# Optimization experiments

Measured on AMD Instinct MI355X. Metric: run time of the kernel, lower is better.

Reference implementation:

```python
import jax, jax.numpy as jnp
import numpy as np

N_NODES = 40000
N_EDGES = 640000
IN_CH = 11
HID = 128
OUT_CH = 1
NUM_LEVELS = 2


def _lin(x, w, b):
    # torch nn.Linear: w is [out, in]
    return x @ w.T + b


def _conv(x, src, dst, w1, b1, w2, b2, w3, b3):
    # Reconstructed MLMPNNConv forward: embed, then NUM_LEVELS rounds of
    # scatter-add message passing (message = x_j), concat levels, project.
    h = jax.nn.relu(_lin(x, w1, b1))  # [N, HID]
    outs = []
    for _ in range(NUM_LEVELS):
        agg = jax.ops.segment_sum(h[src], dst, num_segments=N_NODES)  # gather + scatter-add
        h = jax.nn.relu(_lin(agg, w2, b2))
        outs.append(h)
    return _lin(jnp.concatenate(outs, axis=-1), w3, b3)  # [N, out]


def setup_inputs() -> dict:
    key = jax.random.key(0)
    ks = jax.random.split(key, 16)
    d = {}
    d["x"] = jax.random.normal(ks[0], (N_NODES, IN_CH), dtype=jnp.float32)
    d["edge_index"] = jax.random.randint(ks[1], (2, N_EDGES), 0, N_NODES, dtype=jnp.int32)
    s = 0.05
    # conv 0: lin1 IN->HID, lin2 HID->HID, lin3 2*HID->HID
    d["c0_w1"] = jax.random.normal(ks[2], (HID, IN_CH)) * s
    d["c0_b1"] = jnp.zeros((HID,), jnp.float32)
    d["c0_w2"] = jax.random.normal(ks[3], (HID, HID)) * s
    d["c0_b2"] = jnp.zeros((HID,), jnp.float32)
    d["c0_w3"] = jax.random.normal(ks[4], (HID, HID * NUM_LEVELS)) * s
    d["c0_b3"] = jnp.zeros((HID,), jnp.float32)
    # conv 1: lin1 HID->HID
    d["c1_w1"] = jax.random.normal(ks[5], (HID, HID)) * s
    d["c1_b1"] = jnp.zeros((HID,), jnp.float32)
    d["c1_w2"] = jax.random.normal(ks[6], (HID, HID)) * s
    d["c1_b2"] = jnp.zeros((HID,), jnp.float32)
    d["c1_w3"] = jax.random.normal(ks[7], (HID, HID * NUM_LEVELS)) * s
    d["c1_b3"] = jnp.zeros((HID,), jnp.float32)
    # head
    d["f_w1"] = jax.random.normal(ks[8], (HID, HID)) * s
    d["f_b1"] = jnp.zeros((HID,), jnp.float32)
    d["f_w2"] = jax.random.normal(ks[9], (OUT_CH, HID)) * s
    d["f_b2"] = jnp.zeros((OUT_CH,), jnp.float32)
    return d


def reference(x, edge_index,
              c0_w1, c0_b1, c0_w2, c0_b2, c0_w3, c0_b3,
              c1_w1, c1_b1, c1_w2, c1_b2, c1_w3, c1_b3,
              f_w1, f_b1, f_w2, f_b2):
    src, dst = edge_index[0], edge_index[1]
    h = _conv(x, src, dst, c0_w1, c0_b1, c0_w2, c0_b2, c0_w3, c0_b3)
    h = _conv(h, src, dst, c1_w1, c1_b1, c1_w2, c1_b2, c1_w3, c1_b3)
    h = jax.nn.relu(_lin(h, f_w1, f_b1))
    return _lin(h, f_w2, f_b2)  # [N, 1]
```

## Files before the change

kernel.cpp:

```cpp
#include <hip/hip_runtime.h>
#include <hip/hip_fp16.h>

#define NN 40000
#define NE 640000
#define HID 128
#define SCAN_BLK ((NN + 255) / 256)

typedef __attribute__((ext_vector_type(8)))  short short8;
typedef __attribute__((ext_vector_type(4)))  short short4v;
typedef __attribute__((ext_vector_type(16))) float floatx16;
typedef unsigned int uint;

__device__ __forceinline__ short f2bf(float f) {
    union { float f; unsigned u; } c; c.f = f;
    unsigned u = c.u;
    unsigned r = (u + 0x7FFF + ((u >> 16) & 1)) >> 16;
    return (short)r;
}
__device__ __forceinline__ float bf2f(short h) {
    union { unsigned u; float f; } c;
    c.u = ((unsigned)(unsigned short)h) << 16;
    return c.f;
}
__device__ __forceinline__ float2 h2f2(uint u) {
    union { uint u; __half2 h; } c; c.u = u;
    return __half22float2(c.h);
}
__device__ __forceinline__ void splits(float f, short* hi, short* lo) {
    short h = f2bf(f);
    *hi = h;
    *lo = f2bf(f - bf2f(h));
}
__device__ __forceinline__ void unpack8(uint4 a, uint4 b, short8* h, short8* l) {
    short8 H, L;
    H[0] = (short)(a.x >> 16); L[0] = (short)a.x;
    H[1] = (short)(a.y >> 16); L[1] = (short)a.y;
    H[2] = (short)(a.z >> 16); L[2] = (short)a.z;
    H[3] = (short)(a.w >> 16); L[3] = (short)a.w;
    H[4] = (short)(b.x >> 16); L[4] = (short)b.x;
    H[5] = (short)(b.y >> 16); L[5] = (short)b.y;
    H[6] = (short)(b.z >> 16); L[6] = (short)b.z;
    H[7] = (short)(b.w >> 16); L[7] = (short)b.w;
    *h = H; *l = L;
}

__device__ __forceinline__ int wswz(int o, int k) {
    int chunk = k >> 4, half = (k >> 3) & 1, j = k & 7;
    int ct = o >> 5, m31 = o & 31;
    int lane = half * 32 + m31;
    return (((chunk * 4 + ct) * 64 + lane) * 8 + j);
}

#define ACCH(u, A)                                      \
    { float2 f0 = h2f2(u.x), f1 = h2f2(u.y);            \
      A.x += f0.x; A.y += f0.y; A.z += f1.x; A.w += f1.y; }

__global__ __launch_bounds__(256, 4) void fused_gather_lin_kernel(
    const __half* __restrict__ h, const int* __restrict__ row_ptr,
    const int* __restrict__ esrc, const uint* __restrict__ Wq,
    const float* __restrict__ bias, __half* __restrict__ out)
{
    __shared__ short sAh[4096];
    __shared__ short sAl[4096];
    const int t  = threadIdx.x;
    const int r0 = blockIdx.x * 32;
    const int c4 = t & 31;
    const int sub = c4 >> 1;
    const int j0  = (c4 & 1) * 4;
    const uint2* hp = (const uint2*)h;

    for (int p = 0; p < 4; ++p) {
        const int nl   = p * 8 + (t >> 5);
        const int node = r0 + nl;
        const int lo = row_ptr[node], hi = row_ptr[node + 1];
        float4 a = make_float4(0,0,0,0), b = make_float4(0,0,0,0);
        float4 c = make_float4(0,0,0,0), d = make_float4(0,0,0,0);
        int e = lo;
        for (; e + 4 <= hi; e += 4) {
            int s0 = esrc[e], s1 = esrc[e+1], s2 = esrc[e+2], s3 = esrc[e+3];
            uint2 u0 = hp[(size_t)s0 * 32 + c4];
            uint2 u1 = hp[(size_t)s1 * 32 + c4];
            uint2 u2 = hp[(size_t)s2 * 32 + c4];
            uint2 u3 = hp[(size_t)s3 * 32 + c4];
            ACCH(u0, a); ACCH(u1, b); ACCH(u2, c); ACCH(u3, d);
        }
        for (; e < hi; ++e) {
            int s0 = esrc[e];
            uint2 u0 = hp[(size_t)s0 * 32 + c4];
            ACCH(u0, a);
        }
        float vx = (a.x + b.x) + (c.x + d.x);
        float vy = (a.y + b.y) + (c.y + d.y);
        float vz = (a.z + b.z) + (c.z + d.z);
        float vw = (a.w + b.w) + (c.w + d.w);
        short4v Hq, Lq;
        short hh, ll;
        splits(vx, &hh, &ll); Hq.x = hh; Lq.x = ll;
        splits(vy, &hh, &ll); Hq.y = hh; Lq.y = ll;
        splits(vz, &hh, &ll); Hq.z = hh; Lq.z = ll;
        splits(vw, &hh, &ll); Hq.w = hh; Lq.w = ll;
        const int off = sub * 256 + nl * 8 + j0;
        *(short4v*)(sAh + off) = Hq;
        *(short4v*)(sAl + off) = Lq;
    }
    __syncthreads();

    const int wv   = t >> 6;
    const int lane = t & 63;
    const int m31  = lane & 31;
    const int half = lane >> 5;
    floatx16 acc;
    #pragma unroll
    for (int i = 0; i < 16; ++i) acc[i] = 0.f;
    #pragma unroll
    for (int c = 0; c < 8; ++c) {
        short8 ah = *(const short8*)(sAh + (c * 2 + half) * 256 + m31 * 8);
        short8 al = *(const short8*)(sAl + (c * 2 + half) * 256 + m31 * 8);
        const uint* wr = Wq + ((size_t)(c * 4 + wv) * 64 + lane) * 8;
        uint4 w0 = *(const uint4*)(wr);
        uint4 w1 = *(const uint4*)(wr + 4);
        short8 bh, bl;
        unpack8(w0, w1, &bh, &bl);
        acc = __builtin_amdgcn_mfma_f32_32x32x16_bf16(ah, bh, acc, 0, 0, 0);
        acc = __builtin_amdgcn_mfma_f32_32x32x16_bf16(al, bh, acc, 0, 0, 0);
        acc = __builtin_amdgcn_mfma_f32_32x32x16_bf16(ah, bl, acc, 0, 0, 0);
    }
    const int col = wv * 32 + m31;
    const float bb = bias[col];
    #pragma unroll
    for (int reg = 0; reg < 16; ++reg) {
        int row = (reg & 3) + 8 * (reg >> 2) + 4 * half;
        float v = fmaxf(acc[reg] + bb, 0.f);
        out[(size_t)(r0 + row) * HID + col] = __float2half(v);
    }
}

template<int PHASES, bool RELU>
__global__ __launch_bounds__(256, 4) void lin32_kernel(
    const __half* __restrict__ X0, const __half* __restrict__ X1,
    const uint* __restrict__ Wq, const float* __restrict__ bias,
    __half* __restrict__ out)
{
    __shared__ short sAh[PHASES * 4096];
    __shared__ short sAl[PHASES * 4096];
    const int t  = threadIdx.x;
    const int r0 = blockIdx.x * 32;

    #pragma unroll
    for (int i = 0; i < PHASES * 4; ++i) {
        int v = t + 256 * i;
        const __half* Xp = (PHASES == 2 && v >= 1024) ? X1 : X0;
        int vv  = v & 1023;
        int row = vv >> 5, q = vv & 31;
        uint2 u = *(const uint2*)(Xp + (size_t)(r0 + row) * 128 + q * 4);
        float2 f0 = h2f2(u.x), f1 = h2f2(u.y);
        int kk  = ((PHASES == 2) ? (v >> 10) * 128 : 0) + q * 4;
        int off = (kk >> 3) * 256 + row * 8 + (q & 1) * 4;
        short4v hi, lo;
        short hh, ll;
        splits(f0.x, &hh, &ll); hi.x = hh; lo.x = ll;
        splits(f0.y, &hh, &ll); hi.y = hh; lo.y = ll;
        splits(f1.x, &hh, &ll); hi.z = hh; lo.z = ll;
        splits(f1.y, &hh, &ll); hi.w = hh; lo.w = ll;
        *(short4v*)(sAh + off) = hi;
        *(short4v*)(sAl + off) = lo;
    }
    __syncthreads();

    const int wv   = t >> 6;
    const int lane = t & 63;
    const int m31  = lane & 31;
    const int half = lane >> 5;
    floatx16 acc;
    #pragma unroll
    for (int i = 0; i < 16; ++i) acc[i] = 0.f;
    #pragma unroll
    for (int c = 0; c < PHASES * 8; ++c) {
        short8 ah = *(const short8*)(sAh + (c * 2 + half) * 256 + m31 * 8);
        short8 al = *(const short8*)(sAl + (c * 2 + half) * 256 + m31 * 8);
        const uint* wr = Wq + ((size_t)(c * 4 + wv) * 64 + lane) * 8;
        uint4 w0 = *(const uint4*)(wr);
        uint4 w1 = *(const uint4*)(wr + 4);
        short8 bh, bl;
        unpack8(w0, w1, &bh, &bl);
        acc = __builtin_amdgcn_mfma_f32_32x32x16_bf16(ah, bh, acc, 0, 0, 0);
        acc = __builtin_amdgcn_mfma_f32_32x32x16_bf16(al, bh, acc, 0, 0, 0);
        acc = __builtin_amdgcn_mfma_f32_32x32x16_bf16(ah, bl, acc, 0, 0, 0);
    }
    const int col = wv * 32 + m31;
    const float bb = bias[col];
    #pragma unroll
    for (int reg = 0; reg < 16; ++reg) {
        int row = (reg & 3) + 8 * (reg >> 2) + 4 * half;
        float v = acc[reg] + bb;
        if (RELU) v = fmaxf(v, 0.f);
        out[(size_t)(r0 + row) * HID + col] = __float2half(v);
    }
}

__global__ __launch_bounds__(256, 3) void cat_head_kernel(
    const __half* __restrict__ X0, const __half* __restrict__ X1,
    const uint* __restrict__ Wq, const float* __restrict__ bias,
    const float* __restrict__ f2, const float* __restrict__ f2b,
    float* __restrict__ out)
{
    __shared__ short sAh[8192];
    __shared__ short sAl[8192];
    __shared__ float gbuf[32 * 129];
    const int t  = threadIdx.x;
    const int r0 = blockIdx.x * 32;

    #pragma unroll
    for (int i = 0; i < 8; ++i) {
        int v = t + 256 * i;
        const __half* Xp = (v >= 1024) ? X1 : X0;
        int vv  = v & 1023;
        int row = vv >> 5, q = vv & 31;
        uint2 u = *(const uint2*)(Xp + (size_t)(r0 + row) * 128 + q * 4);
        float2 f0 = h2f2(u.x), f1 = h2f2(u.y);
        int kk  = (v >> 10) * 128 + q * 4;
        int off = (kk >> 3) * 256 + row * 8 + (q & 1) * 4;
        short4v hi, lo;
        short hh, ll;
        splits(f0.x, &hh, &ll); hi.x = hh; lo.x = ll;
        splits(f0.y, &hh, &ll); hi.y = hh; lo.y = ll;
        splits(f1.x, &hh, &ll); hi.z = hh; lo.z = ll;
        splits(f1.y, &hh, &ll); hi.w = hh; lo.w = ll;
        *(short4v*)(sAh + off) = hi;
        *(short4v*)(sAl + off) = lo;
    }
    __syncthreads();

    const int wv   = t >> 6;
    const int lane = t & 63;
    const int m31  = lane & 31;
    const int half = lane >> 5;
    floatx16 acc;
    #pragma unroll
    for (int i = 0; i < 16; ++i) acc[i] = 0.f;
    #pragma unroll
    for (int c = 0; c < 16; ++c) {
        short8 ah = *(const short8*)(sAh + (c * 2 + half) * 256 + m31 * 8);
        short8 al = *(const short8*)(sAl + (c * 2 + half) * 256 + m31 * 8);
        const uint* wr = Wq + ((size_t)(c * 4 + wv) * 64 + lane) * 8;
        uint4 w0 = *(const uint4*)(wr);
        uint4 w1 = *(const uint4*)(wr + 4);
        short8 bh, bl;
        unpack8(w0, w1, &bh, &bl);
        acc = __builtin_amdgcn_mfma_f32_32x32x16_bf16(ah, bh, acc, 0, 0, 0);
        acc = __builtin_amdgcn_mfma_f32_32x32x16_bf16(al, bh, acc, 0, 0, 0);
        acc = __builtin_amdgcn_mfma_f32_32x32x16_bf16(ah, bl, acc, 0, 0, 0);
    }
    const int col = wv * 32 + m31;
    const float bb = bias[col];
    #pragma unroll
    for (int reg = 0; reg < 16; ++reg) {
        int row = (reg & 3) + 8 * (reg >> 2) + 4 * half;
        gbuf[row * 129 + col] = fmaxf(acc[reg] + bb, 0.f);
    }
    __syncthreads();

    const int node = t >> 3;
    const int seg  = t & 7;
    const float* gr = gbuf + node * 129 + seg * 16;
    float a = 0.f;
    #pragma unroll
    for (int i = 0; i < 16; ++i) a += gr[i] * f2[seg * 16 + i];
    a += __shfl_down(a, 4, 8);
    a += __shfl_down(a, 2, 8);
    a += __shfl_down(a, 1, 8);
    if (seg == 0) out[r0 + node] = a + f2b[0];
}

template<int K, bool RELU>
__global__ __launch_bounds__(128) void lin_kernel(
    const float* __restrict__ X, const float* __restrict__ W,
    const float* __restrict__ b, __half* __restrict__ out, int n_rows)
{
    constexpr int ROWS = 8;
    __shared__ float xs[ROWS * K];
    const int m  = threadIdx.x;
    const int r0 = blockIdx.x * ROWS;
    for (int i = threadIdx.x; i < ROWS * K; i += 128) {
        int r = i / K, k = i - r * K;
        int row = r0 + r;
        xs[i] = (row < n_rows) ? X[(size_t)row * K + k] : 0.f;
    }
    __syncthreads();
    float acc[ROWS] = {};
    const float* Wm = W + (size_t)m * K;
    for (int k = 0; k < K; ++k) {
        float w = Wm[k];
        #pragma unroll
        for (int r = 0; r < ROWS; ++r) acc[r] += xs[r * K + k] * w;
    }
    const float bias = b[m];
    #pragma unroll
    for (int r = 0; r < ROWS; ++r) {
        int row = r0 + r;
        if (row < n_rows) {
            float v = acc[r] + bias;
            if (RELU) v = fmaxf(v, 0.f);
            out[(size_t)row * HID + m] = __float2half(v);
        }
    }
}

__global__ __launch_bounds__(256) void wprep_kernel(
    const float* __restrict__ w0, const float* __restrict__ w1,
    uint* __restrict__ wp)
{
    int i = blockIdx.x * 256 + threadIdx.x;
    if (i >= 32768) return;
    const float* src = (i < 16384) ? w0 : w1;
    int off = (i < 16384) ? 0 : 16384;
    int L = i - off;
    int o = L >> 7, k = L & 127;
    float f = src[L];
    short hh, ll;
    splits(f, &hh, &ll);
    wp[off + wswz(o, k)] = ((uint)(unsigned short)hh << 16) | (uint)(unsigned short)ll;
}

__global__ __launch_bounds__(256) void wfold_kernel(
    const float* __restrict__ A, const float* __restrict__ B,
    const float* __restrict__ b_in, const float* __restrict__ b_out,
    uint* __restrict__ outWq, float* __restrict__ outBias)
{
    const int o = blockIdx.x;
    const int k = threadIdx.x;
    const float* Ar = A + o * 128;
    float s = 0.f;
    for (int j = 0; j < 128; ++j) s += Ar[j] * B[j * 256 + k];
    short hh, ll;
    splits(s, &hh, &ll);
    outWq[wswz(o, k)] = ((uint)(unsigned short)hh << 16) | (uint)(unsigned short)ll;
    if (k == 0) {
        float sb = 0.f;
        for (int j = 0; j < 128; ++j) sb += Ar[j] * b_in[j];
        outBias[o] = sb + b_out[o];
    }
}

__global__ __launch_bounds__(256) void hist_kernel(
    const int* __restrict__ dst, int* __restrict__ cnt)
{
    int e = blockIdx.x * 256 + threadIdx.x;
    if (e < NE) atomicAdd(&cnt[dst[e]], 1);
}

__global__ __launch_bounds__(256) void scan1_kernel(
    const int* __restrict__ cnt, int* __restrict__ row_ptr,
    int* __restrict__ partials)
{
    __shared__ int s[256];
    const int t = threadIdx.x;
    const int i = blockIdx.x * 256 + t;
    int v = (i < NN) ? cnt[i] : 0;
    s[t] = v;
    __syncthreads();
    #pragma unroll
    for (int off = 1; off < 256; off <<= 1) {
        int x = (t >= off) ? s[t - off] : 0;
        __syncthreads();
        s[t] += x;
        __syncthreads();
    }
    if (i < NN) row_ptr[i] = s[t] - v;
    if (t == 255) partials[blockIdx.x] = s[255];
}

__global__ __launch_bounds__(256) void scan2_kernel(
    int* __restrict__ partials, int* __restrict__ row_ptr)
{
    __shared__ int s[256];
    const int t = threadIdx.x;
    int v = (t < SCAN_BLK) ? partials[t] : 0;
    s[t] = v;
    __syncthreads();
    #pragma unroll
    for (int off = 1; off < 256; off <<= 1) {
        int x = (t >= off) ? s[t - off] : 0;
        __syncthreads();
        s[t] += x;
        __syncthreads();
    }
    if (t < SCAN_BLK) partials[t] = s[t] - v;
    if (t == 255) row_ptr[NN] = s[255];
}

__global__ __launch_bounds__(256) void scan3_kernel(
    int* __restrict__ row_ptr, const int* __restrict__ partials)
{
    const int i = blockIdx.x * 256 + threadIdx.x;
    if (i < NN) row_ptr[i] += partials[blockIdx.x];
}

__global__ __launch_bounds__(256) void fill_kernel(
    const int* __restrict__ src, const int* __restrict__ dst,
    const int* __restrict__ row_ptr, int* __restrict__ pos,
    int* __restrict__ esrc)
{
    int e = blockIdx.x * 256 + threadIdx.x;
    if (e >= NE) return;
    int d = dst[e];
    int p = row_ptr[d] + atomicAdd(&pos[d], 1);
    esrc[p] = src[e];
}

extern "C" void kernel_launch(void* const* d_in, const int* in_sizes, int n_in,
                              void* d_out, int out_size, void* d_ws, size_t ws_size,
                              hipStream_t stream)
{
    const float* x     = (const float*)d_in[0];
    const int*   eidx  = (const int*)d_in[1];
    const float* c0_w1 = (const float*)d_in[2],  *c0_b1 = (const float*)d_in[3];
    const float* c0_w2 = (const float*)d_in[4],  *c0_b2 = (const float*)d_in[5];
    const float* c0_w3 = (const float*)d_in[6],  *c0_b3 = (const float*)d_in[7];
    const float* c1_w1 = (const float*)d_in[8],  *c1_b1 = (const float*)d_in[9];
    const float* c1_w2 = (const float*)d_in[10], *c1_b2 = (const float*)d_in[11];
    const float* c1_w3 = (const float*)d_in[12], *c1_b3 = (const float*)d_in[13];
    const float* f_w1  = (const float*)d_in[14], *f_b1  = (const float*)d_in[15];
    const float* f_w2  = (const float*)d_in[16], *f_b2  = (const float*)d_in[17];
    const int* src = eidx;
    const int* dst = eidx + NE;
    float* out = (float*)d_out;

    const size_t BUF = (size_t)NN * HID;
    __half* bA = (__half*)d_ws;
    __half* bB = bA + BUF;
    __half* bC = bB + BUF;
    int* row_ptr  = (int*)(bC + BUF);
    int* cnt      = row_ptr + (NN + 1);
    int* pos      = cnt + NN;
    int* esrc     = pos + NN;
    int* partials = esrc + NE;
    uint* wp      = (uint*)(partials + SCAN_BLK);

    uint* p_c0w2 = wp + 0;
    uint* p_c1w2 = wp + 16384;
    uint* p_Wa   = wp + 32768;
    uint* p_Wb   = wp + 65536;
    float* f_ba  = (float*)(wp + 98304);
    float* f_bb  = f_ba + 128;

    const int nb8 = (NN + 7) / 8;
    const int nbl = (NN + 31) / 32;
    const int eb  = (NE + 255) / 256;

    wprep_kernel<<<128, 256, 0, stream>>>(c0_w2, c1_w2, wp);
    wfold_kernel<<<128, 256, 0, stream>>>(c1_w1, c0_w3, c0_b3, c1_b1, p_Wa, f_ba);
    wfold_kernel<<<128, 256, 0, stream>>>(f_w1, c1_w3, c1_b3, f_b1, p_Wb, f_bb);
    (void)hipMemsetAsync(cnt, 0, 2 * NN * sizeof(int), stream);
    hist_kernel<<<eb, 256, 0, stream>>>(dst, cnt);
    scan1_kernel<<<SCAN_BLK, 256, 0, stream>>>(cnt, row_ptr, partials);
    scan2_kernel<<<1, 256, 0, stream>>>(partials, row_ptr);
    scan3_kernel<<<SCAN_BLK, 256, 0, stream>>>(row_ptr, partials);
    fill_kernel<<<eb, 256, 0, stream>>>(src, dst, row_ptr, pos, esrc);

    lin_kernel<11, true><<<nb8, 128, 0, stream>>>(x, c0_w1, c0_b1, bA, NN);
    fused_gather_lin_kernel<<<nbl, 256, 0, stream>>>(bA, row_ptr, esrc, p_c0w2, c0_b2, bB);
    fused_gather_lin_kernel<<<nbl, 256, 0, stream>>>(bB, row_ptr, esrc, p_c0w2, c0_b2, bC);
    lin32_kernel<2, true><<<nbl, 256, 0, stream>>>(bB, bC, p_Wa, f_ba, bA);

    fused_gather_lin_kernel<<<nbl, 256, 0, stream>>>(bA, row_ptr, esrc, p_c1w2, c1_b2, bB);
    fused_gather_lin_kernel<<<nbl, 256, 0, stream>>>(bB, row_ptr, esrc, p_c1w2, c1_b2, bC);
    cat_head_kernel<<<nbl, 256, 0, stream>>>(bB, bC, p_Wb, f_bb, f_w2, f_b2, out);
}
```

Measured before the change: 344.6 us.

## Merge setup kernels and balance gather rows with a shared-memory work counter

The weight prep, the two weight-fold kernels and the degree histogram now run as one launch split by block index. The edge fill and the input embedding linear layer also share one launch. This removes several launches and lets independent work overlap. Inside the fused gather kernel, each 32-lane group now takes node rows from a shared atomic counter instead of a fixed set of four rows, so the uneven node degrees are spread across groups more evenly. The cost is an extra barrier and a shared atomic per row.

```diff
diff --git a/kernel.cpp b/kernel.cpp
--- a/kernel.cpp
+++ b/kernel.cpp
@@ -5,6 +5,7 @@
 #define NE 640000
 #define HID 128
 #define SCAN_BLK ((NN + 255) / 256)
+#define EB ((NE + 255) / 256)
 
 typedef __attribute__((ext_vector_type(8)))  short short8;
 typedef __attribute__((ext_vector_type(4)))  short short4v;
@@ -62,6 +63,7 @@
 {
     __shared__ short sAh[4096];
     __shared__ short sAl[4096];
+    __shared__ int   sCtr;
     const int t  = threadIdx.x;
     const int r0 = blockIdx.x * 32;
     const int c4 = t & 31;
@@ -69,9 +71,15 @@
     const int j0  = (c4 & 1) * 4;
     const uint2* hp = (const uint2*)h;
 
-    for (int p = 0; p < 4; ++p) {
-        const int nl   = p * 8 + (t >> 5);
-        const int node = r0 + nl;
+    if (t == 0) sCtr = 0;
+    __syncthreads();
+
+    for (;;) {
+        int n = 0;
+        if ((t & 31) == 0) n = atomicAdd(&sCtr, 1);
+        n = __shfl(n, 0, 32);
+        if (n >= 32) break;
+        const int node = r0 + n;
         const int lo = row_ptr[node], hi = row_ptr[node + 1];
         float4 a = make_float4(0,0,0,0), b = make_float4(0,0,0,0);
         float4 c = make_float4(0,0,0,0), d = make_float4(0,0,0,0);
@@ -99,7 +107,7 @@
         splits(vy, &hh, &ll); Hq.y = hh; Lq.y = ll;
         splits(vz, &hh, &ll); Hq.z = hh; Lq.z = ll;
         splits(vw, &hh, &ll); Hq.w = hh; Lq.w = ll;
-        const int off = sub * 256 + nl * 8 + j0;
+        const int off = sub * 256 + n * 8 + j0;
         *(short4v*)(sAh + off) = Hq;
         *(short4v*)(sAl + off) = Lq;
     }
@@ -272,81 +280,51 @@
     if (seg == 0) out[r0 + node] = a + f2b[0];
 }
 
-template<int K, bool RELU>
-__global__ __launch_bounds__(128) void lin_kernel(
-    const float* __restrict__ X, const float* __restrict__ W,
-    const float* __restrict__ b, __half* __restrict__ out, int n_rows)
-{
-    constexpr int ROWS = 8;
-    __shared__ float xs[ROWS * K];
-    const int m  = threadIdx.x;
-    const int r0 = blockIdx.x * ROWS;
-    for (int i = threadIdx.x; i < ROWS * K; i += 128) {
-        int r = i / K, k = i - r * K;
-        int row = r0 + r;
-        xs[i] = (row < n_rows) ? X[(size_t)row * K + k] : 0.f;
-    }
-    __syncthreads();
-    float acc[ROWS] = {};
-    const float* Wm = W + (size_t)m * K;
-    for (int k = 0; k < K; ++k) {
-        float w = Wm[k];
-        #pragma unroll
-        for (int r = 0; r < ROWS; ++r) acc[r] += xs[r * K + k] * w;
-    }
-    const float bias = b[m];
-    #pragma unroll
-    for (int r = 0; r < ROWS; ++r) {
-        int row = r0 + r;
-        if (row < n_rows) {
-            float v = acc[r] + bias;
-            if (RELU) v = fmaxf(v, 0.f);
-            out[(size_t)row * HID + m] = __float2half(v);
-        }
-    }
-}
-
-__global__ __launch_bounds__(256) void wprep_kernel(
-    const float* __restrict__ w0, const float* __restrict__ w1,
-    uint* __restrict__ wp)
-{
-    int i = blockIdx.x * 256 + threadIdx.x;
-    if (i >= 32768) return;
-    const float* src = (i < 16384) ? w0 : w1;
-    int off = (i < 16384) ? 0 : 16384;
-    int L = i - off;
-    int o = L >> 7, k = L & 127;
-    float f = src[L];
-    short hh, ll;
-    splits(f, &hh, &ll);
-    wp[off + wswz(o, k)] = ((uint)(unsigned short)hh << 16) | (uint)(unsigned short)ll;
-}
-
-__global__ __launch_bounds__(256) void wfold_kernel(
-    const float* __restrict__ A, const float* __restrict__ B,
-    const float* __restrict__ b_in, const float* __restrict__ b_out,
-    uint* __restrict__ outWq, float* __restrict__ outBias)
-{
-    const int o = blockIdx.x;
-    const int k = threadIdx.x;
-    const float* Ar = A + o * 128;
-    float s = 0.f;
-    for (int j = 0; j < 128; ++j) s += Ar[j] * B[j * 256 + k];
-    short hh, ll;
-    splits(s, &hh, &ll);
-    outWq[wswz(o, k)] = ((uint)(unsigned short)hh << 16) | (uint)(unsigned short)ll;
-    if (k == 0) {
-        float sb = 0.f;
-        for (int j = 0; j < 128; ++j) sb += Ar[j] * b_in[j];
-        outBias[o] = sb + b_out[o];
-    }
-}
-
-__global__ __launch_bounds__(256) void hist_kernel(
-    const int* __restrict__ dst, int* __restrict__ cnt)
-{
-    int e = blockIdx.x * 256 + threadIdx.x;
-    if (e < NE) atomicAdd(&cnt[dst[e]], 1);
+__global__ __launch_bounds__(256) void prep_kernel(
+    const float* __restrict__ c0w2, const float* __restrict__ c1w2,
+    const float* __restrict__ c1w1, const float* __restrict__ c0w3,
+    const float* __restrict__ c0b3, const float* __restrict__ c1b1,
+    const float* __restrict__ fw1,  const float* __restrict__ c1w3,
+    const float* __restrict__ c1b3, const float* __restrict__ fb1,
+    const int* __restrict__ dst, int* __restrict__ cnt,
+    uint* __restrict__ wp, uint* __restrict__ p_Wa, uint* __restrict__ p_Wb,
+    float* __restrict__ f_ba, float* __restrict__ f_bb)
+{
+    const int b = blockIdx.x;
+    const int t = threadIdx.x;
+    if (b < 128) {
+        int i = b * 256 + t;
+        const float* src = (i < 16384) ? c0w2 : c1w2;
+        int off = (i < 16384) ? 0 : 16384;
+        int L = i - off;
+        int o = L >> 7, k = L & 127;
+        short hh, ll;
+        splits(src[L], &hh, &ll);
+        wp[off + wswz(o, k)] = ((uint)(unsigned short)hh << 16) | (uint)(unsigned short)ll;
+    } else if (b < 384) {
+        const bool isA = (b < 256);
+        const int o = b - (isA ? 128 : 256);
+        const float* A   = isA ? c1w1 : fw1;
+        const float* B   = isA ? c0w3 : c1w3;
+        const float* bi  = isA ? c0b3 : c1b3;
+        const float* bo  = isA ? c1b1 : fb1;
+        uint*  W  = isA ? p_Wa : p_Wb;
+        float* bb = isA ? f_ba : f_bb;
+        const float* Ar = A + o * 128;
+        float s = 0.f;
+        for (int j = 0; j < 128; ++j) s += Ar[j] * B[j * 256 + t];
+        short hh, ll;
+        splits(s, &hh, &ll);
+        W[wswz(o, t)] = ((uint)(unsigned short)hh << 16) | (uint)(unsigned short)ll;
+        if (t == 0) {
+            float sb = 0.f;
+            for (int j = 0; j < 128; ++j) sb += Ar[j] * bi[j];
+            bb[o] = sb + bo[o];
+        }
+    } else {
+        int e = (b - 384) * 256 + t;
+        if (e < NE) atomicAdd(&cnt[dst[e]], 1);
+    }
 }
 
 __global__ __launch_bounds__(256) void scan1_kernel(
@@ -396,16 +374,47 @@
     if (i < NN) row_ptr[i] += partials[blockIdx.x];
 }
 
-__global__ __launch_bounds__(256) void fill_kernel(
+__global__ __launch_bounds__(256) void fill_embed_kernel(
     const int* __restrict__ src, const int* __restrict__ dst,
     const int* __restrict__ row_ptr, int* __restrict__ pos,
-    int* __restrict__ esrc)
-{
-    int e = blockIdx.x * 256 + threadIdx.x;
-    if (e >= NE) return;
-    int d = dst[e];
-    int p = row_ptr[d] + atomicAdd(&pos[d], 1);
-    esrc[p] = src[e];
+    int* __restrict__ esrc,
+    const float* __restrict__ x, const float* __restrict__ w1,
+    const float* __restrict__ b1, __half* __restrict__ h0)
+{
+    const int b = blockIdx.x;
+    const int t = threadIdx.x;
+    if (b < EB) {
+        int e = b * 256 + t;
+        if (e < NE) {
+            int d = dst[e];
+            int p = row_ptr[d] + atomicAdd(&pos[d], 1);
+            esrc[p] = src[e];
+        }
+    } else {
+        __shared__ float xs[2][88];
+        const int hf = t >> 7;
+        const int m  = t & 127;
+        const int r0 = (b - EB) * 16 + hf * 8;
+        for (int i = m; i < 88; i += 128) {
+            int r = i / 11, k = i - r * 11;
+            xs[hf][i] = x[(size_t)(r0 + r) * 11 + k];
+        }
+        __syncthreads();
+        float acc[8] = {};
+        const float* Wm = w1 + m * 11;
+        #pragma unroll
+        for (int k = 0; k < 11; ++k) {
+            float w = Wm[k];
+            #pragma unroll
+            for (int r = 0; r < 8; ++r) acc[r] += xs[hf][r * 11 + k] * w;
+        }
+        const float bias = b1[m];
+        #pragma unroll
+        for (int r = 0; r < 8; ++r) {
+            float v = fmaxf(acc[r] + bias, 0.f);
+            h0[(size_t)(r0 + r) * HID + m] = __float2half(v);
+        }
+    }
 }
 
 extern "C" void kernel_launch(void* const* d_in, const int* in_sizes, int n_in,
@@ -444,21 +453,18 @@
     float* f_ba  = (float*)(wp + 98304);
     float* f_bb  = f_ba + 128;
 
-    const int nb8 = (NN + 7) / 8;
     const int nbl = (NN + 31) / 32;
-    const int eb  = (NE + 255) / 256;
-
-    wprep_kernel<<<128, 256, 0, stream>>>(c0_w2, c1_w2, wp);
-    wfold_kernel<<<128, 256, 0, stream>>>(c1_w1, c0_w3, c0_b3, c1_b1, p_Wa, f_ba);
-    wfold_kernel<<<128, 256, 0, stream>>>(f_w1, c1_w3, c1_b3, f_b1, p_Wb, f_bb);
+
     (void)hipMemsetAsync(cnt, 0, 2 * NN * sizeof(int), stream);
-    hist_kernel<<<eb, 256, 0, stream>>>(dst, cnt);
+    prep_kernel<<<384 + EB, 256, 0, stream>>>(
+        c0_w2, c1_w2, c1_w1, c0_w3, c0_b3, c1_b1,
+        f_w1, c1_w3, c1_b3, f_b1, dst, cnt, wp, p_Wa, p_Wb, f_ba, f_bb);
     scan1_kernel<<<SCAN_BLK, 256, 0, stream>>>(cnt, row_ptr, partials);
     scan2_kernel<<<1, 256, 0, stream>>>(partials, row_ptr);
     scan3_kernel<<<SCAN_BLK, 256, 0, stream>>>(row_ptr, partials);
-    fill_kernel<<<eb, 256, 0, stream>>>(src, dst, row_ptr, pos, esrc);
-
-    lin_kernel<11, true><<<nb8, 128, 0, stream>>>(x, c0_w1, c0_b1, bA, NN);
+    fill_embed_kernel<<<EB + 2500, 256, 0, stream>>>(
+        src, dst, row_ptr, pos, esrc, x, c0_w1, c0_b1, bA);
+
     fused_gather_lin_kernel<<<nbl, 256, 0, stream>>>(bA, row_ptr, esrc, p_c0w2, c0_b2, bB);
     fused_gather_lin_kernel<<<nbl, 256, 0, stream>>>(bB, row_ptr, esrc, p_c0w2, c0_b2, bC);
     lin32_kernel<2, true><<<nbl, 256, 0, stream>>>(bB, bC, p_Wa, f_ba, bA);
```

Measured after the change: 331.1 us. 1.04x faster.
